# Kernel tuning notes

Measured on AMD Instinct MI355X. Metric: run time of the kernel, lower is better.

The kernel has to match this reference:

```python
import jax, jax.numpy as jnp
import numpy as np

B, T, H, I = 256, 1024, 512, 1


def _uniform(key, shape, bound):
    return jax.random.uniform(key, shape, jnp.float32, -bound, bound)


def setup_inputs() -> dict:
    key = jax.random.key(0)
    ks = jax.random.split(key, 11)
    s = 1.0 / np.sqrt(H)
    return {
        "input": jax.random.normal(ks[0], (B, T), jnp.float32),
        "W_ih1": _uniform(ks[1], (3 * H, I), s),
        "W_hh1": _uniform(ks[2], (3 * H, H), s),
        "b_ih1": _uniform(ks[3], (3 * H,), s),
        "b_hh1": _uniform(ks[4], (3 * H,), s),
        "W_ih2": _uniform(ks[5], (3 * H, H), s),
        "W_hh2": _uniform(ks[6], (3 * H, H), s),
        "b_ih2": _uniform(ks[7], (3 * H,), s),
        "b_hh2": _uniform(ks[8], (3 * H,), s),
        "W_out": _uniform(ks[9], (1, H), s),
        "b_out": _uniform(ks[10], (1,), s),
        "future": 0,
    }


def _gru_cell(x, h, W_ih, W_hh, b_ih, b_hh):
    # PyTorch nn.GRUCell: gates ordered (r, z, n)
    gi = x @ W_ih.T + b_ih          # [B, 3H]
    gh = h @ W_hh.T + b_hh          # [B, 3H]
    i_r, i_z, i_n = jnp.split(gi, 3, axis=-1)
    h_r, h_z, h_n = jnp.split(gh, 3, axis=-1)
    r = jax.nn.sigmoid(i_r + h_r)
    z = jax.nn.sigmoid(i_z + h_z)
    n = jnp.tanh(i_n + r * h_n)
    return (1.0 - z) * n + z * h


def _run(input, W_ih1, W_hh1, b_ih1, b_hh1, W_ih2, W_hh2, b_ih2, b_hh2, W_out, b_out, future):
    Bb = input.shape[0]
    h0 = jnp.zeros((Bb, H), input.dtype)

    def step(carry, x_t):  # x_t: [B]
        h1, h2 = carry
        h1 = _gru_cell(x_t[:, None], h1, W_ih1, W_hh1, b_ih1, b_hh1)
        h2 = _gru_cell(h1, h2, W_ih2, W_hh2, b_ih2, b_hh2)
        out = h2 @ W_out.T + b_out  # [B, 1]
        return (h1, h2), out[:, 0]

    (h1, h2), ys = jax.lax.scan(step, (h0, h0), input.T)  # ys: [T, B]
    outs = [ys.T]  # [B, T]
    out = ys[-1][:, None]
    for _ in range(future):
        (h1, h2), o = step((h1, h2), out[:, 0])
        out = o[:, None]
        outs.append(out)
    return jnp.concatenate(outs, axis=1) if future > 0 else outs[0]


def reference(input, W_ih1, W_hh1, b_ih1, b_hh1, W_ih2, W_hh2, b_ih2, b_hh2, W_out, b_out, future):
    return _run(input, W_ih1, W_hh1, b_ih1, b_hh1, W_ih2, W_hh2, b_ih2, b_hh2, W_out, b_out, future)
```

## Files before the change

### kernel.cpp

```cpp
#include <hip/hip_runtime.h>

#define NB 256
#define NT 512
#define TT 1024
#define HH 512
#define BATCH 256
#define UB 16
#define BGB 32

using v8s   = __attribute__((ext_vector_type(8))) short;
using f32x4 = __attribute__((ext_vector_type(4))) float;

#define O_STG  0
#define O_N1   32768
#define O_WOUT 65536
#define O_ZERO 67584
#define O_SCR  67600
#define O_SO   113680
#define LDS_BYTES 113936

#define SLOT_SH 524288

__device__ __forceinline__ float sigf(float v)   { return 1.f / (1.f + __expf(-v)); }
__device__ __forceinline__ float tanhf_(float v) { return 2.f / (1.f + __expf(-2.f * v)) - 1.f; }

__device__ __forceinline__ unsigned short bf16_rne(float f) {
    union { float f; unsigned u; } a; a.f = f;
    unsigned r = (a.u + 0x7fffu + ((a.u >> 16) & 1u)) >> 16;
    return (unsigned short)r;
}
__device__ __forceinline__ float bf16_f(unsigned short h) {
    union { unsigned u; float f; } a; a.u = ((unsigned)h) << 16; return a.f;
}
__device__ __forceinline__ f32x4 MF(v8s a, v8s b, f32x4 c) {
    return __builtin_amdgcn_mfma_f32_16x16x32_bf16(a, b, c, 0, 0, 0);
}
#define T3(ACC, AH_, AL_, BH_, BL_) \
    ACC = MF(AH_, BH_, ACC); ACC = MF(AL_, BH_, ACC); ACC = MF(AH_, BL_, ACC);

#define GST2(addr, val) \
    asm volatile("global_store_short %0, %1, off sc0 sc1" \
                 :: "v"(addr), "v"((unsigned)(val)) : "memory");

__device__ __forceinline__ void gridbar(unsigned* barr, int bg, int tid,
                                        unsigned ep, bool fence) {
    asm volatile("s_waitcnt vmcnt(0)" ::: "memory");
    __syncthreads();
    if (tid == 0) {
        unsigned* cnt = barr + bg * 64;
        __hip_atomic_fetch_add(cnt, 1u, __ATOMIC_RELAXED, __HIP_MEMORY_SCOPE_AGENT);
        while (__hip_atomic_load(cnt, __ATOMIC_RELAXED, __HIP_MEMORY_SCOPE_AGENT) < ep * 32u)
            __builtin_amdgcn_s_sleep(1);
        if (fence)
            __builtin_amdgcn_fence(__ATOMIC_ACQUIRE, "agent");
    }
    __syncthreads();
}

__global__ __launch_bounds__(256) void k_transpose(const float* __restrict__ x,
                                                   float* __restrict__ xT) {
    __shared__ float tile[64][65];
    const int bt = blockIdx.x, bb = blockIdx.y;
    const int lt = threadIdx.x & 63, lb = threadIdx.x >> 6;
    #pragma unroll 4
    for (int i = 0; i < 16; ++i) {
        int row = lb + i * 4;
        tile[row][lt] = x[(size_t)(bb * 64 + row) * TT + bt * 64 + lt];
    }
    __syncthreads();
    #pragma unroll 4
    for (int i = 0; i < 16; ++i) {
        int row = lb + i * 4;
        xT[(size_t)(bt * 64 + row) * BATCH + bb * 64 + lt] = tile[lt][row];
    }
}

#define STAGE_TILE(SRC) \
    for (int i = tid; i < 16 * 512; i += NT) { \
        int n = i >> 9, k = i & 511; \
        float f = (SRC)[(size_t)(u0 + n) * HH + k]; \
        unsigned short hi = bf16_rne(f), lo = bf16_rne(f - bf16_f(hi)); \
        int s = k >> 5, g = (k >> 3) & 3, j = k & 7, ln = g * 16 + n; \
        int base = O_STG + s * 2048 + ln * 16 + j * 2; \
        *(unsigned short*)(lds_b + base) = hi; \
        *(unsigned short*)(lds_b + base + 1024) = lo; }

#define GRAB(RB) { \
    const char* bp = lds_b + O_STG + lane * 16; \
    _Pragma("unroll") for (int s8 = 0; s8 < 8; ++s8) { \
        RB[s8][0] = *(const v8s*)(bp + (kh * 8 + s8) * 2048); \
        RB[s8][1] = *(const v8s*)(bp + (kh * 8 + s8) * 2048 + 1024); } }

#define PUB(TAU, A0, A1v) \
    _Pragma("unroll") for (int j = 0; j < 4; ++j) { \
        sk[(TAU) * 640 + (g4 * 4 + j) * 20 + n16]      = (A0)[j]; \
        sk[(TAU) * 640 + (16 + g4 * 4 + j) * 20 + n16] = (A1v)[j]; }

__global__ __launch_bounds__(NT, 1) void gru_mfma(
    const float* __restrict__ xT,
    const float* __restrict__ Wih1, const float* __restrict__ Whh1,
    const float* __restrict__ bih1, const float* __restrict__ bhh1,
    const float* __restrict__ Wih2, const float* __restrict__ Whh2,
    const float* __restrict__ bih2, const float* __restrict__ bhh2,
    const float* __restrict__ Wout, const float* __restrict__ bout,
    float* __restrict__ out,
    unsigned short* __restrict__ hws,
    unsigned* __restrict__ barr,
    int rmask, int invmask)
{
    extern __shared__ char lds_b[];
    const int tid = threadIdx.x, blk = blockIdx.x;

    const int bg   = blk >> 5;
    const int slot = blk & 31;
    const int u0   = slot * UB;
    const bool doOut = (slot == 0);

    const int w = tid >> 6, lane = tid & 63;
    const int n16 = lane & 15, g4 = lane >> 4;
    const int kh = w & 1, tg = w >> 1;

    if (tid < 4) ((unsigned*)(lds_b + O_ZERO))[tid] = 0;
    v8s RB0[8][2], RB1[8][2];
    const size_t G = (size_t)HH * HH;
    STAGE_TILE(Whh2)          __syncthreads(); if (tg == 0) GRAB(RB0) __syncthreads();
    STAGE_TILE(Whh2 + G)      __syncthreads(); if (tg == 0) GRAB(RB1) __syncthreads();
    STAGE_TILE(Wih2)          __syncthreads(); if (tg == 1) GRAB(RB0) __syncthreads();
    STAGE_TILE(Wih2 + G)      __syncthreads(); if (tg == 1) GRAB(RB1) __syncthreads();
    STAGE_TILE(Wih2 + 2 * G)  __syncthreads(); if (tg == 2) GRAB(RB0) __syncthreads();
    STAGE_TILE(Whh2 + 2 * G)  __syncthreads(); if (tg == 2) GRAB(RB1) __syncthreads();
    STAGE_TILE(Whh1)          __syncthreads(); if (tg == 3) GRAB(RB0) __syncthreads();
    STAGE_TILE(Whh1 + G)      __syncthreads(); if (tg == 3) GRAB(RB1) __syncthreads();
    for (int i = tid; i < 16 * 512; i += NT) {
        int n = i >> 9, k = i & 511;
        float f = Whh1[2 * G + (size_t)(u0 + n) * HH + k];
        unsigned short hi = bf16_rne(f), lo = bf16_rne(f - bf16_f(hi));
        int s = k >> 5, g = (k >> 3) & 3, j = k & 7, ln = g * 16 + n;
        int base = O_N1 + s * 2048 + ln * 16 + j * 2;
        *(unsigned short*)(lds_b + base) = hi;
        *(unsigned short*)(lds_b + base + 1024) = lo;
    }
    for (int k = tid; k < 512; k += NT) {
        float f = Wout[k];
        unsigned short hi = bf16_rne(f), lo = bf16_rne(f - bf16_f(hi));
        int s = k >> 5, g = (k >> 3) & 3, j = k & 7;
        int base = O_WOUT + s * 64 + g * 16 + j * 2;
        *(unsigned short*)(lds_b + base) = hi;
        *(unsigned short*)(lds_b + base + 1024) = lo;
    }

    const int u = tid & 15, b = tid >> 4;
    const int gu = u0 + u;
    const int gb = bg * BGB + b;
    const float b2r  = bih2[gu] + bhh2[gu];
    const float b2z  = bih2[HH + gu] + bhh2[HH + gu];
    const float b2in = bih2[2 * HH + gu], b2hn = bhh2[2 * HH + gu];
    const float w1r = Wih1[gu], w1z = Wih1[HH + gu], w1n = Wih1[2 * HH + gu];
    const float b1r = bih1[gu] + bhh1[gu];
    const float b1z = bih1[HH + gu] + bhh1[HH + gu];
    const float b1ni = bih1[2 * HH + gu], b1nh = bhh1[2 * HH + gu];
    const float bo = bout[0];

    float h1prev, h2prev = 0.f;
    {
        unsigned short* s0 = hws + (size_t)bg * 65536;
        float x0 = xT[gb];
        float r = sigf(x0 * w1r + b1r);
        float z = sigf(x0 * w1z + b1z);
        float n = tanhf_(x0 * w1n + b1ni + r * b1nh);
        h1prev = (1.f - z) * n;
        unsigned short hi = bf16_rne(h1prev), lo = bf16_rne(h1prev - bf16_f(hi));
        GST2(s0 + (size_t)b * 512 + gu, hi);
        GST2(s0 + 16384 + (size_t)b * 512 + gu, lo);
        GST2(s0 + 32768 + (size_t)b * 512 + gu, 0u);
        GST2(s0 + 49152 + (size_t)b * 512 + gu, 0u);
    }

    const char* n1p  = lds_b + O_N1 + lane * 16;
    const char* BoP  = (n16 == 0) ? lds_b + O_WOUT + kh * 512 + g4 * 16
                                  : lds_b + O_ZERO;
    const char* BolP = (n16 == 0) ? BoP + 1024 : lds_b + O_ZERO;
    const int bos = (n16 == 0) ? 64 : 0;
    float* sk = (float*)(lds_b + O_SCR) + kh * 5760;

    const int rowA = n16 * 512 + kh * 256 + g4 * 8;

    unsigned ep = 1;
    gridbar(barr, bg, tid, ep, true);

    for (int t = 0; t <= TT; ++t) {
        const unsigned short* __restrict__ setR =
            hws + (size_t)(t & rmask) * SLOT_SH + (size_t)bg * 65536;
        unsigned short* __restrict__ setW =
            hws + (size_t)((t + 1) & rmask) * SLOT_SH + (size_t)bg * 65536;

        const unsigned short* __restrict__ p1h0 = setR + rowA;
        const unsigned short* __restrict__ p1h1 = p1h0 + 8192;
        const unsigned short* __restrict__ p1l0 = setR + 16384 + rowA;
        const unsigned short* __restrict__ p1l1 = p1l0 + 8192;
        const unsigned short* __restrict__ p2h0 = setR + 32768 + rowA;
        const unsigned short* __restrict__ p2h1 = p2h0 + 8192;
        const unsigned short* __restrict__ p2l0 = setR + 49152 + rowA;
        const unsigned short* __restrict__ p2l1 = p2l0 + 8192;

        f32x4 acc[2][2];
        #pragma unroll
        for (int m = 0; m < 2; ++m)
            #pragma unroll
            for (int q = 0; q < 2; ++q) acc[m][q] = (f32x4){0.f, 0.f, 0.f, 0.f};
        f32x4 ao[2] = {{0.f,0.f,0.f,0.f}, {0.f,0.f,0.f,0.f}};

        if (tg == 0) {
            #pragma unroll
            for (int sl = 0; sl < 8; ++sl) {
                const v8s a0h = *(const v8s*)(p2h0 + sl * 32);
                const v8s a0l = *(const v8s*)(p2l0 + sl * 32);
                const v8s a1h = *(const v8s*)(p2h1 + sl * 32);
                const v8s a1l = *(const v8s*)(p2l1 + sl * 32);
                T3(acc[0][0], a0h, a0l, RB0[sl][0], RB0[sl][1])
                T3(acc[1][0], a1h, a1l, RB0[sl][0], RB0[sl][1])
                T3(acc[0][1], a0h, a0l, RB1[sl][0], RB1[sl][1])
                T3(acc[1][1], a1h, a1l, RB1[sl][0], RB1[sl][1])
                if (doOut) {
                    v8s wh = *(const v8s*)(BoP + sl * bos);
                    v8s wl = *(const v8s*)(BolP + sl * bos);
                    T3(ao[0], a0h, a0l, wh, wl)
                    T3(ao[1], a1h, a1l, wh, wl)
                }
            }
            PUB(3, acc[0][0], acc[1][0])
            PUB(4, acc[0][1], acc[1][1])
            if (doOut && n16 == 0) {
                float* sp = (float*)(lds_b + O_SO) + kh * 32;
                #pragma unroll
                for (int j = 0; j < 4; ++j) {
                    sp[g4 * 4 + j]      = ao[0][j];
                    sp[16 + g4 * 4 + j] = ao[1][j];
                }
            }
        } else if (tg == 1) {
            #pragma unroll
            for (int sl = 0; sl < 8; ++sl) {
                const v8s a0h = *(const v8s*)(p1h0 + sl * 32);
                const v8s a0l = *(const v8s*)(p1l0 + sl * 32);
                const v8s a1h = *(const v8s*)(p1h1 + sl * 32);
                const v8s a1l = *(const v8s*)(p1l1 + sl * 32);
                T3(acc[0][0], a0h, a0l, RB0[sl][0], RB0[sl][1])
                T3(acc[1][0], a1h, a1l, RB0[sl][0], RB0[sl][1])
                T3(acc[0][1], a0h, a0l, RB1[sl][0], RB1[sl][1])
                T3(acc[1][1], a1h, a1l, RB1[sl][0], RB1[sl][1])
            }
            PUB(0, acc[0][0], acc[1][0])
            PUB(1, acc[0][1], acc[1][1])
        } else if (tg == 2) {
            #pragma unroll
            for (int sl = 0; sl < 8; ++sl) {
                const v8s a0h = *(const v8s*)(p1h0 + sl * 32);
                const v8s a0l = *(const v8s*)(p1l0 + sl * 32);
                const v8s a1h = *(const v8s*)(p1h1 + sl * 32);
                const v8s a1l = *(const v8s*)(p1l1 + sl * 32);
                T3(acc[0][0], a0h, a0l, RB0[sl][0], RB0[sl][1])
                T3(acc[1][0], a1h, a1l, RB0[sl][0], RB0[sl][1])
                const v8s c0h = *(const v8s*)(p2h0 + sl * 32);
                const v8s c0l = *(const v8s*)(p2l0 + sl * 32);
                const v8s c1h = *(const v8s*)(p2h1 + sl * 32);
                const v8s c1l = *(const v8s*)(p2l1 + sl * 32);
                T3(acc[0][1], c0h, c0l, RB1[sl][0], RB1[sl][1])
                T3(acc[1][1], c1h, c1l, RB1[sl][0], RB1[sl][1])
            }
            PUB(2, acc[0][0], acc[1][0])
            PUB(5, acc[0][1], acc[1][1])
        } else {
            f32x4 an[2] = {{0.f,0.f,0.f,0.f}, {0.f,0.f,0.f,0.f}};
            #pragma unroll
            for (int sl = 0; sl < 8; ++sl) {
                const v8s a0h = *(const v8s*)(p1h0 + sl * 32);
                const v8s a0l = *(const v8s*)(p1l0 + sl * 32);
                const v8s a1h = *(const v8s*)(p1h1 + sl * 32);
                const v8s a1l = *(const v8s*)(p1l1 + sl * 32);
                T3(acc[0][0], a0h, a0l, RB0[sl][0], RB0[sl][1])
                T3(acc[1][0], a1h, a1l, RB0[sl][0], RB0[sl][1])
                T3(acc[0][1], a0h, a0l, RB1[sl][0], RB1[sl][1])
                T3(acc[1][1], a1h, a1l, RB1[sl][0], RB1[sl][1])
                const v8s nh = *(const v8s*)(n1p + (kh * 8 + sl) * 2048);
                const v8s nl = *(const v8s*)(n1p + (kh * 8 + sl) * 2048 + 1024);
                T3(an[0], a0h, a0l, nh, nl)
                T3(an[1], a1h, a1l, nh, nl)
            }
            PUB(6, acc[0][0], acc[1][0])
            PUB(7, acc[0][1], acc[1][1])
            PUB(8, an[0], an[1])
        }
        __syncthreads();

        {
            const float* sA = (const float*)(lds_b + O_SCR);
            const float* sB = sA + 5760;
            const int ei = b * 20 + u;
            float v0 = sA[0 * 640 + ei] + sB[0 * 640 + ei];
            float v1 = sA[1 * 640 + ei] + sB[1 * 640 + ei];
            float v2 = sA[2 * 640 + ei] + sB[2 * 640 + ei];
            float v3 = sA[3 * 640 + ei] + sB[3 * 640 + ei];
            float v4 = sA[4 * 640 + ei] + sB[4 * 640 + ei];
            float v5 = sA[5 * 640 + ei] + sB[5 * 640 + ei];
            float v6 = sA[6 * 640 + ei] + sB[6 * 640 + ei];
            float v7 = sA[7 * 640 + ei] + sB[7 * 640 + ei];
            float v8 = sA[8 * 640 + ei] + sB[8 * 640 + ei];

            float r2 = sigf(v0 + v3 + b2r);
            float z2 = sigf(v1 + v4 + b2z);
            float n2 = tanhf_(v2 + b2in + r2 * (v5 + b2hn));
            float h2n = (1.f - z2) * n2 + z2 * h2prev;
            if (t < TT) {
                h2prev = h2n;
                unsigned short hi = bf16_rne(h2n), lo = bf16_rne(h2n - bf16_f(hi));
                GST2(setW + 32768 + (size_t)b * 512 + gu, hi);
                GST2(setW + 49152 + (size_t)b * 512 + gu, lo);
            }
            float xv = (t + 1 < TT) ? xT[(size_t)(t + 1) * BATCH + gb] : 0.f;
            float r1 = sigf(xv * w1r + v6 + b1r);
            float z1 = sigf(xv * w1z + v7 + b1z);
            float n1 = tanhf_(xv * w1n + b1ni + r1 * (v8 + b1nh));
            float h1n = (1.f - z1) * n1 + z1 * h1prev;
            if (t + 1 < TT) {
                h1prev = h1n;
                unsigned short hi = bf16_rne(h1n), lo = bf16_rne(h1n - bf16_f(hi));
                GST2(setW + (size_t)b * 512 + gu, hi);
                GST2(setW + 16384 + (size_t)b * 512 + gu, lo);
            }
            if (doOut && u == 0 && t >= 1) {
                const float* sp = (const float*)(lds_b + O_SO);
                out[(size_t)gb * TT + (t - 1)] = sp[b] + sp[32 + b] + bo;
            }
        }
        ++ep;
        gridbar(barr, bg, tid, ep, (t & invmask) == invmask);
    }
}

extern "C" void kernel_launch(void* const* d_in, const int* in_sizes, int n_in,
                              void* d_out, int out_size, void* d_ws, size_t ws_size,
                              hipStream_t stream) {
    const float* x    = (const float*)d_in[0];
    const float* Wih1 = (const float*)d_in[1];
    const float* Whh1 = (const float*)d_in[2];
    const float* bih1 = (const float*)d_in[3];
    const float* bhh1 = (const float*)d_in[4];
    const float* Wih2 = (const float*)d_in[5];
    const float* Whh2 = (const float*)d_in[6];
    const float* bih2 = (const float*)d_in[7];
    const float* bhh2 = (const float*)d_in[8];
    const float* Wout = (const float*)d_in[9];
    const float* bout = (const float*)d_in[10];
    float* outp = (float*)d_out;

    const size_t MB = 1048576;
    size_t avail = (ws_size > MB + 8192) ? ws_size - MB - 8192 : 2 * MB;
    int R = 2;
    while (R < 64 && (size_t)(R * 2) * MB <= avail) R *= 2;
    const int INVP = (R >= 4) ? (R / 2) : 1;

    unsigned short* hws = (unsigned short*)d_ws;
    float* xTp     = (float*)((char*)d_ws + (size_t)R * MB);
    unsigned* barr = (unsigned*)((char*)d_ws + (size_t)R * MB + MB);

    hipMemsetAsync((void*)barr, 0, 8192, stream);
    k_transpose<<<dim3(16, 4), 256, 0, stream>>>(x, xTp);

    hipFuncSetAttribute((const void*)gru_mfma,
                        hipFuncAttributeMaxDynamicSharedMemorySize, LDS_BYTES);

    int rmask = R - 1, invmask = INVP - 1;
    void* args[] = { (void*)&xTp,
                     (void*)&Wih1, (void*)&Whh1, (void*)&bih1, (void*)&bhh1,
                     (void*)&Wih2, (void*)&Whh2, (void*)&bih2, (void*)&bhh2,
                     (void*)&Wout, (void*)&bout,
                     (void*)&outp, (void*)&hws, (void*)&barr,
                     (void*)&rmask, (void*)&invmask };
    hipLaunchCooperativeKernel((void*)gru_mfma, dim3(NB), dim3(NT),
                               args, LDS_BYTES, stream);
}
```

Before: 12.22 ms.

## Split each block's batch group into two halves with ping-pong split-phase barriers

Each block now handles two 16-row batch subgroups in alternation, and the grid barrier is split into separate arrive and wait steps with one counter per subgroup. While a block waits for the other blocks to finish subgroup A, it can compute subgroup B, which is meant to hide barrier latency behind useful work. LDS scratch shrinks and now overlaps the staging region. The cost is smaller MFMA tiles per phase, twice as many barrier operations per step, and a harder-to-follow synchronisation protocol.

```diff
diff --git a/kernel.cpp b/kernel.cpp
--- a/kernel.cpp
+++ b/kernel.cpp
@@ -6,18 +6,18 @@
 #define HH 512
 #define BATCH 256
 #define UB 16
-#define BGB 32
+#define BGB 16
 
 using v8s   = __attribute__((ext_vector_type(8))) short;
 using f32x4 = __attribute__((ext_vector_type(4))) float;
 
 #define O_STG  0
+#define O_SCR  0
+#define O_SO   23040
 #define O_N1   32768
 #define O_WOUT 65536
 #define O_ZERO 67584
-#define O_SCR  67600
-#define O_SO   113680
-#define LDS_BYTES 113936
+#define LDS_BYTES 67600
 
 #define SLOT_SH 524288
 
@@ -42,14 +42,15 @@
     asm volatile("global_store_short %0, %1, off sc0 sc1" \
                  :: "v"(addr), "v"((unsigned)(val)) : "memory");
 
-__device__ __forceinline__ void gridbar(unsigned* barr, int bg, int tid,
-                                        unsigned ep, bool fence) {
+__device__ __forceinline__ void bar_arrive(unsigned* cnt, int tid) {
     asm volatile("s_waitcnt vmcnt(0)" ::: "memory");
     __syncthreads();
+    if (tid == 0)
+        __hip_atomic_fetch_add(cnt, 1u, __ATOMIC_RELAXED, __HIP_MEMORY_SCOPE_AGENT);
+}
+__device__ __forceinline__ void bar_wait(unsigned* cnt, int tid, unsigned target, bool fence) {
     if (tid == 0) {
-        unsigned* cnt = barr + bg * 64;
-        __hip_atomic_fetch_add(cnt, 1u, __ATOMIC_RELAXED, __HIP_MEMORY_SCOPE_AGENT);
-        while (__hip_atomic_load(cnt, __ATOMIC_RELAXED, __HIP_MEMORY_SCOPE_AGENT) < ep * 32u)
+        while (__hip_atomic_load(cnt, __ATOMIC_RELAXED, __HIP_MEMORY_SCOPE_AGENT) < target)
             __builtin_amdgcn_s_sleep(1);
         if (fence)
             __builtin_amdgcn_fence(__ATOMIC_ACQUIRE, "agent");
@@ -91,10 +92,112 @@
         RB[s8][0] = *(const v8s*)(bp + (kh * 8 + s8) * 2048); \
         RB[s8][1] = *(const v8s*)(bp + (kh * 8 + s8) * 2048 + 1024); } }
 
-#define PUB(TAU, A0, A1v) \
-    _Pragma("unroll") for (int j = 0; j < 4; ++j) { \
-        sk[(TAU) * 640 + (g4 * 4 + j) * 20 + n16]      = (A0)[j]; \
-        sk[(TAU) * 640 + (16 + g4 * 4 + j) * 20 + n16] = (A1v)[j]; }
+#define PUB(TAU, A0) \
+    _Pragma("unroll") for (int j = 0; j < 4; ++j) \
+        sk[(TAU) * 320 + (g4 * 4 + j) * 20 + n16] = (A0)[j];
+
+#define PHASE(BGI, H1PV, H2PV, GBV, CNTP)                                          \
+{                                                                                  \
+    const unsigned short* __restrict__ setR =                                      \
+        hws + (size_t)(t & rmask) * SLOT_SH + (size_t)(BGI) * 32768;               \
+    unsigned short* __restrict__ setW =                                            \
+        hws + (size_t)((t + 1) & rmask) * SLOT_SH + (size_t)(BGI) * 32768;         \
+    const unsigned short* __restrict__ p1h = setR + rowA;                          \
+    const unsigned short* __restrict__ p1l = setR + 8192 + rowA;                   \
+    const unsigned short* __restrict__ p2h = setR + 16384 + rowA;                  \
+    const unsigned short* __restrict__ p2l = setR + 24576 + rowA;                  \
+    f32x4 ac0 = {0.f,0.f,0.f,0.f}, ac1 = {0.f,0.f,0.f,0.f};                        \
+    if (tg == 0) {                                                                 \
+        f32x4 ao0 = {0.f,0.f,0.f,0.f};                                             \
+        _Pragma("unroll") for (int sl = 0; sl < 8; ++sl) {                         \
+            const v8s ah_ = *(const v8s*)(p2h + sl * 32);                          \
+            const v8s al_ = *(const v8s*)(p2l + sl * 32);                          \
+            T3(ac0, ah_, al_, RB0[sl][0], RB0[sl][1])                              \
+            T3(ac1, ah_, al_, RB1[sl][0], RB1[sl][1])                              \
+            if (doOut) {                                                           \
+                v8s wh = *(const v8s*)(BoP + sl * bos);                            \
+                v8s wl = *(const v8s*)(BolP + sl * bos);                           \
+                T3(ao0, ah_, al_, wh, wl)                                          \
+            }                                                                      \
+        }                                                                          \
+        PUB(3, ac0) PUB(4, ac1)                                                    \
+        if (doOut && n16 == 0) {                                                   \
+            float* sp = (float*)(lds_b + O_SO) + kh * 16;                          \
+            _Pragma("unroll") for (int j = 0; j < 4; ++j) sp[g4 * 4 + j] = ao0[j]; \
+        }                                                                          \
+    } else if (tg == 1) {                                                          \
+        _Pragma("unroll") for (int sl = 0; sl < 8; ++sl) {                         \
+            const v8s ah_ = *(const v8s*)(p1h + sl * 32);                          \
+            const v8s al_ = *(const v8s*)(p1l + sl * 32);                          \
+            T3(ac0, ah_, al_, RB0[sl][0], RB0[sl][1])                              \
+            T3(ac1, ah_, al_, RB1[sl][0], RB1[sl][1])                              \
+        }                                                                          \
+        PUB(0, ac0) PUB(1, ac1)                                                    \
+    } else if (tg == 2) {                                                          \
+        _Pragma("unroll") for (int sl = 0; sl < 8; ++sl) {                         \
+            const v8s ah_ = *(const v8s*)(p1h + sl * 32);                          \
+            const v8s al_ = *(const v8s*)(p1l + sl * 32);                          \
+            T3(ac0, ah_, al_, RB0[sl][0], RB0[sl][1])                              \
+            const v8s ch_ = *(const v8s*)(p2h + sl * 32);                          \
+            const v8s cl_ = *(const v8s*)(p2l + sl * 32);                          \
+            T3(ac1, ch_, cl_, RB1[sl][0], RB1[sl][1])                              \
+        }                                                                          \
+        PUB(2, ac0) PUB(5, ac1)                                                    \
+    } else {                                                                       \
+        f32x4 an0 = {0.f,0.f,0.f,0.f};                                             \
+        _Pragma("unroll") for (int sl = 0; sl < 8; ++sl) {                         \
+            const v8s ah_ = *(const v8s*)(p1h + sl * 32);                          \
+            const v8s al_ = *(const v8s*)(p1l + sl * 32);                          \
+            T3(ac0, ah_, al_, RB0[sl][0], RB0[sl][1])                              \
+            T3(ac1, ah_, al_, RB1[sl][0], RB1[sl][1])                              \
+            const v8s nh = *(const v8s*)(n1p + (kh * 8 + sl) * 2048);              \
+            const v8s nl = *(const v8s*)(n1p + (kh * 8 + sl) * 2048 + 1024);       \
+            T3(an0, ah_, al_, nh, nl)                                              \
+        }                                                                          \
+        PUB(6, ac0) PUB(7, ac1) PUB(8, an0)                                        \
+    }                                                                              \
+    __syncthreads();                                                               \
+    if (tid < 256) {                                                               \
+        const float* sA = (const float*)(lds_b + O_SCR);                           \
+        const float* sB = sA + 2880;                                               \
+        const int ei = b * 20 + u;                                                 \
+        float v0 = sA[0 * 320 + ei] + sB[0 * 320 + ei];                            \
+        float v1 = sA[1 * 320 + ei] + sB[1 * 320 + ei];                            \
+        float v2 = sA[2 * 320 + ei] + sB[2 * 320 + ei];                            \
+        float v3 = sA[3 * 320 + ei] + sB[3 * 320 + ei];                            \
+        float v4 = sA[4 * 320 + ei] + sB[4 * 320 + ei];                            \
+        float v5 = sA[5 * 320 + ei] + sB[5 * 320 + ei];                            \
+        float v6 = sA[6 * 320 + ei] + sB[6 * 320 + ei];                            \
+        float v7 = sA[7 * 320 + ei] + sB[7 * 320 + ei];                            \
+        float v8 = sA[8 * 320 + ei] + sB[8 * 320 + ei];                            \
+        float r2 = sigf(v0 + v3 + b2r);                                            \
+        float z2 = sigf(v1 + v4 + b2z);                                            \
+        float n2 = tanhf_(v2 + b2in + r2 * (v5 + b2hn));                           \
+        float h2n = (1.f - z2) * n2 + z2 * (H2PV);                                 \
+        if (t < TT) {                                                              \
+            H2PV = h2n;                                                            \
+            unsigned short hi = bf16_rne(h2n), lo = bf16_rne(h2n - bf16_f(hi));    \
+            GST2(setW + 16384 + (size_t)b * 512 + gu, hi);                         \
+            GST2(setW + 24576 + (size_t)b * 512 + gu, lo);                         \
+        }                                                                          \
+        float xv = (t + 1 < TT) ? xT[(size_t)(t + 1) * BATCH + (GBV)] : 0.f;       \
+        float r1 = sigf(xv * w1r + v6 + b1r);                                      \
+        float z1 = sigf(xv * w1z + v7 + b1z);                                      \
+        float n1 = tanhf_(xv * w1n + b1ni + r1 * (v8 + b1nh));                     \
+        float h1n = (1.f - z1) * n1 + z1 * (H1PV);                                 \
+        if (t + 1 < TT) {                                                          \
+            H1PV = h1n;                                                            \
+            unsigned short hi = bf16_rne(h1n), lo = bf16_rne(h1n - bf16_f(hi));    \
+            GST2(setW + (size_t)b * 512 + gu, hi);                                 \
+            GST2(setW + 8192 + (size_t)b * 512 + gu, lo);                          \
+        }                                                                          \
+        if (doOut && u == 0 && t >= 1) {                                           \
+            const float* sp = (const float*)(lds_b + O_SO);                        \
+            out[(size_t)(GBV) * TT + (t - 1)] = sp[b] + sp[16 + b] + bo;           \
+        }                                                                          \
+    }                                                                              \
+    bar_arrive(CNTP, tid);                                                         \
+}
 
 __global__ __launch_bounds__(NT, 1) void gru_mfma(
     const float* __restrict__ xT,
@@ -111,10 +214,13 @@
     extern __shared__ char lds_b[];
     const int tid = threadIdx.x, blk = blockIdx.x;
 
-    const int bg   = blk >> 5;
+    const int pair = blk >> 5;
     const int slot = blk & 31;
-    const int u0   = slot * UB;
+    const int u0 = slot * UB;
     const bool doOut = (slot == 0);
+    const int bgA = 2 * pair, bgB = 2 * pair + 1;
+    unsigned* cntA = barr + bgA * 64;
+    unsigned* cntB = barr + bgB * 64;
 
     const int w = tid >> 6, lane = tid & 63;
     const int n16 = lane & 15, g4 = lane >> 4;
@@ -149,9 +255,9 @@
         *(unsigned short*)(lds_b + base + 1024) = lo;
     }
 
-    const int u = tid & 15, b = tid >> 4;
+    const int u = tid & 15, b = (tid >> 4) & 15;
     const int gu = u0 + u;
-    const int gb = bg * BGB + b;
+    const int gbA = bgA * BGB + b, gbB = bgB * BGB + b;
     const float b2r  = bih2[gu] + bhh2[gu];
     const float b2z  = bih2[HH + gu] + bhh2[HH + gu];
     const float b2in = bih2[2 * HH + gu], b2hn = bhh2[2 * HH + gu];
@@ -161,19 +267,34 @@
     const float b1ni = bih1[2 * HH + gu], b1nh = bhh1[2 * HH + gu];
     const float bo = bout[0];
 
-    float h1prev, h2prev = 0.f;
-    {
-        unsigned short* s0 = hws + (size_t)bg * 65536;
-        float x0 = xT[gb];
-        float r = sigf(x0 * w1r + b1r);
-        float z = sigf(x0 * w1z + b1z);
-        float n = tanhf_(x0 * w1n + b1ni + r * b1nh);
-        h1prev = (1.f - z) * n;
-        unsigned short hi = bf16_rne(h1prev), lo = bf16_rne(h1prev - bf16_f(hi));
-        GST2(s0 + (size_t)b * 512 + gu, hi);
-        GST2(s0 + 16384 + (size_t)b * 512 + gu, lo);
-        GST2(s0 + 32768 + (size_t)b * 512 + gu, 0u);
-        GST2(s0 + 49152 + (size_t)b * 512 + gu, 0u);
+    float h1A = 0.f, h2A = 0.f, h1B = 0.f, h2B = 0.f;
+    if (tid < 256) {
+        unsigned short* sA0 = hws + (size_t)bgA * 32768;
+        unsigned short* sB0 = hws + (size_t)bgB * 32768;
+        {
+            float x0 = xT[gbA];
+            float r = sigf(x0 * w1r + b1r);
+            float z = sigf(x0 * w1z + b1z);
+            float n = tanhf_(x0 * w1n + b1ni + r * b1nh);
+            h1A = (1.f - z) * n;
+            unsigned short hi = bf16_rne(h1A), lo = bf16_rne(h1A - bf16_f(hi));
+            GST2(sA0 + (size_t)b * 512 + gu, hi);
+            GST2(sA0 + 8192 + (size_t)b * 512 + gu, lo);
+            GST2(sA0 + 16384 + (size_t)b * 512 + gu, 0u);
+            GST2(sA0 + 24576 + (size_t)b * 512 + gu, 0u);
+        }
+        {
+            float x0 = xT[gbB];
+            float r = sigf(x0 * w1r + b1r);
+            float z = sigf(x0 * w1z + b1z);
+            float n = tanhf_(x0 * w1n + b1ni + r * b1nh);
+            h1B = (1.f - z) * n;
+            unsigned short hi = bf16_rne(h1B), lo = bf16_rne(h1B - bf16_f(hi));
+            GST2(sB0 + (size_t)b * 512 + gu, hi);
+            GST2(sB0 + 8192 + (size_t)b * 512 + gu, lo);
+            GST2(sB0 + 16384 + (size_t)b * 512 + gu, 0u);
+            GST2(sB0 + 24576 + (size_t)b * 512 + gu, 0u);
+        }
     }
 
     const char* n1p  = lds_b + O_N1 + lane * 16;
@@ -181,160 +302,19 @@
                                   : lds_b + O_ZERO;
     const char* BolP = (n16 == 0) ? BoP + 1024 : lds_b + O_ZERO;
     const int bos = (n16 == 0) ? 64 : 0;
-    float* sk = (float*)(lds_b + O_SCR) + kh * 5760;
+    float* sk = (float*)(lds_b + O_SCR) + kh * 2880;
 
     const int rowA = n16 * 512 + kh * 256 + g4 * 8;
 
-    unsigned ep = 1;
-    gridbar(barr, bg, tid, ep, true);
+    bar_arrive(cntA, tid);
+    bar_arrive(cntB, tid);
 
     for (int t = 0; t <= TT; ++t) {
-        const unsigned short* __restrict__ setR =
-            hws + (size_t)(t & rmask) * SLOT_SH + (size_t)bg * 65536;
-        unsigned short* __restrict__ setW =
-            hws + (size_t)((t + 1) & rmask) * SLOT_SH + (size_t)bg * 65536;
-
-        const unsigned short* __restrict__ p1h0 = setR + rowA;
-        const unsigned short* __restrict__ p1h1 = p1h0 + 8192;
-        const unsigned short* __restrict__ p1l0 = setR + 16384 + rowA;
-        const unsigned short* __restrict__ p1l1 = p1l0 + 8192;
-        const unsigned short* __restrict__ p2h0 = setR + 32768 + rowA;
-        const unsigned short* __restrict__ p2h1 = p2h0 + 8192;
-        const unsigned short* __restrict__ p2l0 = setR + 49152 + rowA;
-        const unsigned short* __restrict__ p2l1 = p2l0 + 8192;
-
-        f32x4 acc[2][2];
-        #pragma unroll
-        for (int m = 0; m < 2; ++m)
-            #pragma unroll
-            for (int q = 0; q < 2; ++q) acc[m][q] = (f32x4){0.f, 0.f, 0.f, 0.f};
-        f32x4 ao[2] = {{0.f,0.f,0.f,0.f}, {0.f,0.f,0.f,0.f}};
-
-        if (tg == 0) {
-            #pragma unroll
-            for (int sl = 0; sl < 8; ++sl) {
-                const v8s a0h = *(const v8s*)(p2h0 + sl * 32);
-                const v8s a0l = *(const v8s*)(p2l0 + sl * 32);
-                const v8s a1h = *(const v8s*)(p2h1 + sl * 32);
-                const v8s a1l = *(const v8s*)(p2l1 + sl * 32);
-                T3(acc[0][0], a0h, a0l, RB0[sl][0], RB0[sl][1])
-                T3(acc[1][0], a1h, a1l, RB0[sl][0], RB0[sl][1])
-                T3(acc[0][1], a0h, a0l, RB1[sl][0], RB1[sl][1])
-                T3(acc[1][1], a1h, a1l, RB1[sl][0], RB1[sl][1])
-                if (doOut) {
-                    v8s wh = *(const v8s*)(BoP + sl * bos);
-                    v8s wl = *(const v8s*)(BolP + sl * bos);
-                    T3(ao[0], a0h, a0l, wh, wl)
-                    T3(ao[1], a1h, a1l, wh, wl)
-                }
-            }
-            PUB(3, acc[0][0], acc[1][0])
-            PUB(4, acc[0][1], acc[1][1])
-            if (doOut && n16 == 0) {
-                float* sp = (float*)(lds_b + O_SO) + kh * 32;
-                #pragma unroll
-                for (int j = 0; j < 4; ++j) {
-                    sp[g4 * 4 + j]      = ao[0][j];
-                    sp[16 + g4 * 4 + j] = ao[1][j];
-                }
-            }
-        } else if (tg == 1) {
-            #pragma unroll
-            for (int sl = 0; sl < 8; ++sl) {
-                const v8s a0h = *(const v8s*)(p1h0 + sl * 32);
-                const v8s a0l = *(const v8s*)(p1l0 + sl * 32);
-                const v8s a1h = *(const v8s*)(p1h1 + sl * 32);
-                const v8s a1l = *(const v8s*)(p1l1 + sl * 32);
-                T3(acc[0][0], a0h, a0l, RB0[sl][0], RB0[sl][1])
-                T3(acc[1][0], a1h, a1l, RB0[sl][0], RB0[sl][1])
-                T3(acc[0][1], a0h, a0l, RB1[sl][0], RB1[sl][1])
-                T3(acc[1][1], a1h, a1l, RB1[sl][0], RB1[sl][1])
-            }
-            PUB(0, acc[0][0], acc[1][0])
-            PUB(1, acc[0][1], acc[1][1])
-        } else if (tg == 2) {
-            #pragma unroll
-            for (int sl = 0; sl < 8; ++sl) {
-                const v8s a0h = *(const v8s*)(p1h0 + sl * 32);
-                const v8s a0l = *(const v8s*)(p1l0 + sl * 32);
-                const v8s a1h = *(const v8s*)(p1h1 + sl * 32);
-                const v8s a1l = *(const v8s*)(p1l1 + sl * 32);
-                T3(acc[0][0], a0h, a0l, RB0[sl][0], RB0[sl][1])
-                T3(acc[1][0], a1h, a1l, RB0[sl][0], RB0[sl][1])
-                const v8s c0h = *(const v8s*)(p2h0 + sl * 32);
-                const v8s c0l = *(const v8s*)(p2l0 + sl * 32);
-                const v8s c1h = *(const v8s*)(p2h1 + sl * 32);
-                const v8s c1l = *(const v8s*)(p2l1 + sl * 32);
-                T3(acc[0][1], c0h, c0l, RB1[sl][0], RB1[sl][1])
-                T3(acc[1][1], c1h, c1l, RB1[sl][0], RB1[sl][1])
-            }
-            PUB(2, acc[0][0], acc[1][0])
-            PUB(5, acc[0][1], acc[1][1])
-        } else {
-            f32x4 an[2] = {{0.f,0.f,0.f,0.f}, {0.f,0.f,0.f,0.f}};
-            #pragma unroll
-            for (int sl = 0; sl < 8; ++sl) {
-                const v8s a0h = *(const v8s*)(p1h0 + sl * 32);
-                const v8s a0l = *(const v8s*)(p1l0 + sl * 32);
-                const v8s a1h = *(const v8s*)(p1h1 + sl * 32);
-                const v8s a1l = *(const v8s*)(p1l1 + sl * 32);
-                T3(acc[0][0], a0h, a0l, RB0[sl][0], RB0[sl][1])
-                T3(acc[1][0], a1h, a1l, RB0[sl][0], RB0[sl][1])
-                T3(acc[0][1], a0h, a0l, RB1[sl][0], RB1[sl][1])
-                T3(acc[1][1], a1h, a1l, RB1[sl][0], RB1[sl][1])
-                const v8s nh = *(const v8s*)(n1p + (kh * 8 + sl) * 2048);
-                const v8s nl = *(const v8s*)(n1p + (kh * 8 + sl) * 2048 + 1024);
-                T3(an[0], a0h, a0l, nh, nl)
-                T3(an[1], a1h, a1l, nh, nl)
-            }
-            PUB(6, acc[0][0], acc[1][0])
-            PUB(7, acc[0][1], acc[1][1])
-            PUB(8, an[0], an[1])
-        }
-        __syncthreads();
-
-        {
-            const float* sA = (const float*)(lds_b + O_SCR);
-            const float* sB = sA + 5760;
-            const int ei = b * 20 + u;
-            float v0 = sA[0 * 640 + ei] + sB[0 * 640 + ei];
-            float v1 = sA[1 * 640 + ei] + sB[1 * 640 + ei];
-            float v2 = sA[2 * 640 + ei] + sB[2 * 640 + ei];
-            float v3 = sA[3 * 640 + ei] + sB[3 * 640 + ei];
-            float v4 = sA[4 * 640 + ei] + sB[4 * 640 + ei];
-            float v5 = sA[5 * 640 + ei] + sB[5 * 640 + ei];
-            float v6 = sA[6 * 640 + ei] + sB[6 * 640 + ei];
-            float v7 = sA[7 * 640 + ei] + sB[7 * 640 + ei];
-            float v8 = sA[8 * 640 + ei] + sB[8 * 640 + ei];
-
-            float r2 = sigf(v0 + v3 + b2r);
-            float z2 = sigf(v1 + v4 + b2z);
-            float n2 = tanhf_(v2 + b2in + r2 * (v5 + b2hn));
-            float h2n = (1.f - z2) * n2 + z2 * h2prev;
-            if (t < TT) {
-                h2prev = h2n;
-                unsigned short hi = bf16_rne(h2n), lo = bf16_rne(h2n - bf16_f(hi));
-                GST2(setW + 32768 + (size_t)b * 512 + gu, hi);
-                GST2(setW + 49152 + (size_t)b * 512 + gu, lo);
-            }
-            float xv = (t + 1 < TT) ? xT[(size_t)(t + 1) * BATCH + gb] : 0.f;
-            float r1 = sigf(xv * w1r + v6 + b1r);
-            float z1 = sigf(xv * w1z + v7 + b1z);
-            float n1 = tanhf_(xv * w1n + b1ni + r1 * (v8 + b1nh));
-            float h1n = (1.f - z1) * n1 + z1 * h1prev;
-            if (t + 1 < TT) {
-                h1prev = h1n;
-                unsigned short hi = bf16_rne(h1n), lo = bf16_rne(h1n - bf16_f(hi));
-                GST2(setW + (size_t)b * 512 + gu, hi);
-                GST2(setW + 16384 + (size_t)b * 512 + gu, lo);
-            }
-            if (doOut && u == 0 && t >= 1) {
-                const float* sp = (const float*)(lds_b + O_SO);
-                out[(size_t)gb * TT + (t - 1)] = sp[b] + sp[32 + b] + bo;
-            }
-        }
-        ++ep;
-        gridbar(barr, bg, tid, ep, (t & invmask) == invmask);
+        const bool fc = ((t & invmask) == invmask) || (t == 0);
+        bar_wait(cntA, tid, (unsigned)(t + 1) * 32u, fc);
+        PHASE(bgA, h1A, h2A, gbA, cntA)
+        bar_wait(cntB, tid, (unsigned)(t + 1) * 32u, fc);
+        PHASE(bgB, h1B, h2B, gbB, cntB)
     }
 }
 
```

New measurement: 12.86 ms. +5.3%, slower.
